# Kernel tuning notes

Hardware: AMD Instinct MI355X
Metric: run time of the kernel (lower is better)

The kernel has to match this reference:

```python
import jax, jax.numpy as jnp
import numpy as np

D_MODEL = 1024
NUM_HEADS = 16


def setup_inputs() -> dict:
    key = jax.random.key(0)
    ks = jax.random.split(key, 11)
    B, S, D = 2, 2048, D_MODEL
    s = 1.0 / np.sqrt(D)
    return {
        "queries": jax.random.normal(ks[0], (B, S, D), jnp.float32),
        "keys": jax.random.normal(ks[1], (B, S, D), jnp.float32),
        "values": jax.random.normal(ks[2], (B, S, D), jnp.float32),
        "W_q": jax.random.normal(ks[3], (D, D), jnp.float32) * s,
        "b_q": jnp.zeros((D,), jnp.float32),
        "W_k": jax.random.normal(ks[4], (D, D), jnp.float32) * s,
        "b_k": jnp.zeros((D,), jnp.float32),
        "W_v": jax.random.normal(ks[5], (D, D), jnp.float32) * s,
        "b_v": jnp.zeros((D,), jnp.float32),
        "W_o": jax.random.normal(ks[6], (D, D), jnp.float32) * s,
        "b_o": jnp.zeros((D,), jnp.float32),
    }


def _split_heads(x, num_heads):
    # [B, S, D] -> [B, H, S, d_h]
    B, S, D = x.shape
    return x.reshape(B, S, num_heads, D // num_heads).transpose(0, 2, 1, 3)


def reference(queries, keys, values, W_q, b_q, W_k, b_k, W_v, b_v, W_o, b_o):
    H = NUM_HEADS
    Q = _split_heads(queries @ W_q.T + b_q, H)  # [B,H,S,dh]
    K = _split_heads(keys @ W_k.T + b_k, H)
    V = _split_heads(values @ W_v.T + b_v, H)
    d = Q.shape[-1]
    scores = jnp.einsum("bhqd,bhkd->bhqk", Q, K) / jnp.sqrt(jnp.asarray(d, Q.dtype))
    attn = jax.nn.softmax(scores, axis=-1)
    out = jnp.einsum("bhqk,bhkd->bhqd", attn, V)  # [B,H,S,dh]
    B, _, S, _ = out.shape
    out = out.transpose(0, 2, 1, 3).reshape(B, S, -1)  # combine heads
    return out @ W_o.T + b_o
```

## Files before the change

### kernel.cpp

```cpp
#include <hip/hip_runtime.h>
#include <cstdint>
#include <cmath>

typedef short s16x8 __attribute__((ext_vector_type(8)));
typedef short s16x4 __attribute__((ext_vector_type(4)));
typedef float f32x4 __attribute__((ext_vector_type(4)));
typedef unsigned int u32;

#define AS_G __attribute__((address_space(1)))
#define AS_L __attribute__((address_space(3)))

#define QSCALE 0.18033688011112042f

__device__ __forceinline__ void ld16_to_lds(const void* g, const void* l) {
    __builtin_amdgcn_global_load_lds((AS_G void*)(g), (AS_L void*)(l), 16, 0, 0);
}

__device__ __forceinline__ short f2bf(float f) {
    union { float f; uint32_t u; } v; v.f = f;
    uint32_t r = v.u + 0x7fffu + ((v.u >> 16) & 1u);
    return (short)(r >> 16);
}
__device__ __forceinline__ short f2bf_fast(float f) {
    union { float f; uint32_t u; } v; v.f = f;
    return (short)((v.u + 0x8000u) >> 16);
}

template<int F32OUT, int NJ, int QKV>
__global__ __launch_bounds__(256, 3)
void gemm_bt(const short* __restrict__ Abase, long Az,
             const short* __restrict__ Wbase, long Wz,
             const float* __restrict__ bias0, const float* __restrict__ bias1,
             const float* __restrict__ bias2,
             void* __restrict__ Obase, long Oz,
             const int M, const int N, const int K)
{
    constexpr int BN = NJ * 32;
    constexpr int BSt = (BN * 4) / 256;
    constexpr int LPS = 2 + BSt;
    __shared__ __align__(16) short As[3][128 * 32];
    __shared__ __align__(16) short Bs[3][BN * 32];

    const int t = threadIdx.x, lane = t & 63, wv = t >> 6;
    const int wr = wv >> 1, wc = wv & 1;
    const int q4 = lane >> 4, l16 = lane & 15;

    const u32 gx = gridDim.x, gy = gridDim.y;
    u32 lin = blockIdx.x + gx * (blockIdx.y + gy * blockIdx.z);
    const u32 nwg = gx * gy * gridDim.z;
    if ((nwg & 7u) == 0u) lin = (lin & 7u) * (nwg >> 3) + (lin >> 3);
    const int bxs = lin % gx;
    const u32 rem = lin / gx;
    const int bys = rem % gy;
    const int z   = rem / gy;

    const short* A  = Abase + (long)z * Az;
    const short* Bt = Wbase + (long)z * Wz;
    const float* bias = (z == 0) ? bias0 : ((z == 1) ? bias1 : bias2);
    const float bmul = (QKV && z == 0) ? QSCALE : 1.0f;
    const int bn0 = bxs * BN, bm0 = bys * 128;

    f32x4 acc[4][NJ] = {};

    const short* gA[2];
    const short* gB[BSt];
    #pragma unroll
    for (int s = 0; s < 2; ++s) {
        const int c = t + 256 * s;
        const int r = c >> 2, g = (c & 3) ^ ((c >> 3) & 3);
        gA[s] = A + (size_t)(bm0 + r) * K + g * 8;
    }
    #pragma unroll
    for (int s = 0; s < BSt; ++s) {
        const int c = t + 256 * s;
        const int r = c >> 2, g = (c & 3) ^ ((c >> 3) & 3);
        gB[s] = Bt + (size_t)(bn0 + r) * K + g * 8;
    }

    auto stage = [&](int buf) {
        #pragma unroll
        for (int s = 0; s < 2; ++s) {
            ld16_to_lds(gA[s], &As[buf][(wv * 64 + 256 * s) * 8]);
            gA[s] += 32;
        }
        #pragma unroll
        for (int s = 0; s < BSt; ++s) {
            ld16_to_lds(gB[s], &Bs[buf][(wv * 64 + 256 * s) * 8]);
            gB[s] += 32;
        }
    };

    const int kIters = K >> 5;
    stage(0);
    stage(1);
    for (int kt = 0; kt < kIters; ++kt) {
        const int cur = kt % 3;
        if (kt < kIters - 1)
            asm volatile("s_waitcnt vmcnt(%0)" :: "n"(LPS) : "memory");
        else
            asm volatile("s_waitcnt vmcnt(0)" ::: "memory");
        __builtin_amdgcn_s_barrier();
        __builtin_amdgcn_sched_barrier(0);
        if (kt + 2 < kIters) stage((kt + 2) % 3);

        s16x8 aF[4], bF[NJ];
        #pragma unroll
        for (int i = 0; i < 4; ++i) {
            const int m = wr * 64 + i * 16 + l16;
            aF[i] = *(const s16x8*)&As[cur][m * 32 + (q4 ^ ((m >> 1) & 3)) * 8];
        }
        #pragma unroll
        for (int j = 0; j < NJ; ++j) {
            const int n = wc * (BN / 2) + j * 16 + l16;
            bF[j] = *(const s16x8*)&Bs[cur][n * 32 + (q4 ^ ((n >> 1) & 3)) * 8];
        }
        #pragma unroll
        for (int i = 0; i < 4; ++i)
            #pragma unroll
            for (int j = 0; j < NJ; ++j)
                acc[i][j] = __builtin_amdgcn_mfma_f32_16x16x32_bf16(
                    aF[i], bF[j], acc[i][j], 0, 0, 0);
    }

    #pragma unroll
    for (int j = 0; j < NJ; ++j) {
        const int col = bn0 + wc * (BN / 2) + j * 16 + l16;
        const float bj = bias[col] * bmul;
        #pragma unroll
        for (int i = 0; i < 4; ++i) {
            const int row0 = bm0 + wr * 64 + i * 16 + q4 * 4;
            if (QKV && z == 2) {
                s16x4 ov;
                #pragma unroll
                for (int r = 0; r < 4; ++r) ov[r] = f2bf(acc[i][j][r] + bj);
                *(s16x4*)(((short*)Obase + (long)z * Oz) +
                          (size_t)col * 4096 + row0) = ov;
            } else {
                #pragma unroll
                for (int r = 0; r < 4; ++r) {
                    const float v = acc[i][j][r] + bj;
                    if (F32OUT)
                        ((float*)Obase + (long)z * Oz)[(size_t)(row0 + r) * N + col] = v;
                    else
                        ((short*)Obase + (long)z * Oz)[(size_t)(row0 + r) * N + col] = f2bf(v);
                }
            }
        }
    }
}

__global__ __launch_bounds__(256, 2)
void attn_fwd(const short* __restrict__ Qp, const short* __restrict__ Kp,
              const short* __restrict__ VpT, short* __restrict__ Out)
{
    constexpr int D = 1024, S = 2048;
    __shared__ __align__(16) short Ks[2][512 * 8];
    __shared__ __align__(16) short Vt[2][512 * 8];
    __shared__ __align__(16) short Ps[4 * 32 * 72];

    const int t = threadIdx.x, lane = t & 63, wv = t >> 6;
    const int q4 = lane >> 4, l16 = lane & 15;
    const int bid = blockIdx.x;
    const int qt = (bid >> 3) & 15;
    const int hb = (bid & 7) * 4 + (bid >> 7);
    const int h = hb >> 1, b = hb & 1;
    const size_t rowB = (size_t)b * S;
    const int cb = h * 64;
    const int qrow0 = qt * 128 + wv * 32;
    short* PsW = &Ps[wv * (32 * 72)];

    const int ksrow = 4 * l16 + q4;

    s16x8 qF[2][2];
    #pragma unroll
    for (int i = 0; i < 2; ++i)
        #pragma unroll
        for (int tk = 0; tk < 2; ++tk)
            qF[i][tk] = *(const s16x8*)
                &Qp[(rowB + qrow0 + i * 16 + l16) * D + cb + tk * 32 + q4 * 8];

    f32x4 oacc[2][4] = {};
    f32x4 lacc[2] = {};
    s16x8 onesF;
    #pragma unroll
    for (int e = 0; e < 8; ++e) onesF[e] = (short)0x3F80;

    const short* KpB = Kp + rowB * D + cb;
    const short* VtG = VpT + (size_t)cb * 4096 + b * 2048;

    #pragma unroll
    for (int s = 0; s < 2; ++s) {
        ld16_to_lds(KpB + (size_t)ksrow * D + (wv + 4 * s) * 8,
                    &Ks[0][(wv * 64 + 256 * s) * 8]);
    }
    #pragma unroll
    for (int s = 0; s < 2; ++s) {
        const int c = t + 256 * s;
        const int d = c >> 3, kcp = c & 7;
        ld16_to_lds(VtG + (size_t)d * 4096 + ((kcp ^ (d & 7)) * 8),
                    &Vt[0][(wv * 64 + 256 * s) * 8]);
    }

    for (int kvt = 0; kvt < 32; ++kvt) {
        const int kv0 = kvt * 64;
        __syncthreads();
        if (kvt < 31) {
            #pragma unroll
            for (int s = 0; s < 2; ++s) {
                ld16_to_lds(KpB + (size_t)(kv0 + 64 + ksrow) * D + (wv + 4 * s) * 8,
                            &Ks[(kvt + 1) & 1][(wv * 64 + 256 * s) * 8]);
            }
            #pragma unroll
            for (int s = 0; s < 2; ++s) {
                const int c = t + 256 * s;
                const int d = c >> 3, kcp = c & 7;
                ld16_to_lds(VtG + (size_t)d * 4096 + kv0 + 64 + ((kcp ^ (d & 7)) * 8),
                            &Vt[(kvt + 1) & 1][(wv * 64 + 256 * s) * 8]);
            }
        }

        f32x4 acc[2][4] = {};
        #pragma unroll
        for (int tk = 0; tk < 2; ++tk) {
            s16x8 kF[4];
            #pragma unroll
            for (int j = 0; j < 4; ++j)
                kF[j] = *(const s16x8*)
                    &Ks[kvt & 1][((tk * 4 + q4) * 64 + j * 16 + l16) * 8];
            #pragma unroll
            for (int j = 0; j < 4; ++j) {
                acc[0][j] = __builtin_amdgcn_mfma_f32_16x16x32_bf16(
                    qF[0][tk], kF[j], acc[0][j], 0, 0, 0);
                acc[1][j] = __builtin_amdgcn_mfma_f32_16x16x32_bf16(
                    qF[1][tk], kF[j], acc[1][j], 0, 0, 0);
            }
        }

        #pragma unroll
        for (int i = 0; i < 2; ++i) {
            #pragma unroll
            for (int r = 0; r < 4; ++r) {
                const int m = i * 16 + q4 * 4 + r;
                s16x4 pv;
                #pragma unroll
                for (int j = 0; j < 4; ++j)
                    pv[j] = f2bf_fast(__builtin_amdgcn_exp2f(acc[i][j][r]));
                *(s16x4*)&PsW[m * 72 + l16 * 4] = pv;
            }
        }

        #pragma unroll
        for (int tk = 0; tk < 2; ++tk) {
            const s16x8 pF0 = *(const s16x8*)&PsW[l16 * 72 + tk * 32 + q4 * 8];
            const s16x8 pF1 = *(const s16x8*)&PsW[(16 + l16) * 72 + tk * 32 + q4 * 8];
            lacc[0] = __builtin_amdgcn_mfma_f32_16x16x32_bf16(
                pF0, onesF, lacc[0], 0, 0, 0);
            lacc[1] = __builtin_amdgcn_mfma_f32_16x16x32_bf16(
                pF1, onesF, lacc[1], 0, 0, 0);
            #pragma unroll
            for (int jd = 0; jd < 4; ++jd) {
                const int d = jd * 16 + l16;
                const s16x8 vF = *(const s16x8*)
                    &Vt[kvt & 1][(d * 8 + ((tk * 4 + q4) ^ (d & 7))) * 8];
                oacc[0][jd] = __builtin_amdgcn_mfma_f32_16x16x32_bf16(
                    pF0, vF, oacc[0][jd], 0, 0, 0);
                oacc[1][jd] = __builtin_amdgcn_mfma_f32_16x16x32_bf16(
                    pF1, vF, oacc[1][jd], 0, 0, 0);
            }
        }
    }

    #pragma unroll
    for (int i = 0; i < 2; ++i) {
        #pragma unroll
        for (int r = 0; r < 4; ++r) {
            const float inv = 1.0f / lacc[i][r];
            const size_t row = rowB + qrow0 + i * 16 + q4 * 4 + r;
            #pragma unroll
            for (int jd = 0; jd < 4; ++jd)
                Out[row * D + cb + jd * 16 + l16] = f2bf(oacc[i][jd][r] * inv);
        }
    }
}

__global__ __launch_bounds__(256)
void cast_all(const float* __restrict__ q, const float* __restrict__ k,
              const float* __restrict__ v, const float* __restrict__ wq,
              const float* __restrict__ wk, const float* __restrict__ wv,
              const float* __restrict__ wo, short* __restrict__ out)
{
    const size_t i = ((size_t)blockIdx.x * 256 + threadIdx.x) * 8;
    const float* src; size_t off;
    if      (i < 4194304)  { src = q;  off = i; }
    else if (i < 8388608)  { src = k;  off = i - 4194304; }
    else if (i < 12582912) { src = v;  off = i - 8388608; }
    else if (i < 13631488) { src = wq; off = i - 12582912; }
    else if (i < 14680064) { src = wk; off = i - 13631488; }
    else if (i < 15728640) { src = wv; off = i - 14680064; }
    else                   { src = wo; off = i - 15728640; }
    const float m = (i >= 12582912 && i < 13631488) ? QSCALE : 1.0f;
    const float4 a = *(const float4*)(src + off);
    const float4 c = *(const float4*)(src + off + 4);
    s16x8 o;
    o[0] = f2bf(a.x * m); o[1] = f2bf(a.y * m); o[2] = f2bf(a.z * m); o[3] = f2bf(a.w * m);
    o[4] = f2bf(c.x * m); o[5] = f2bf(c.y * m); o[6] = f2bf(c.z * m); o[7] = f2bf(c.w * m);
    *(s16x8*)(out + i) = o;
}

extern "C" void kernel_launch(void* const* d_in, const int* in_sizes, int n_in,
                              void* d_out, int out_size, void* d_ws, size_t ws_size,
                              hipStream_t stream)
{
    const float* q  = (const float*)d_in[0];
    const float* k  = (const float*)d_in[1];
    const float* v  = (const float*)d_in[2];
    const float* Wq = (const float*)d_in[3];
    const float* bq = (const float*)d_in[4];
    const float* Wk = (const float*)d_in[5];
    const float* bk = (const float*)d_in[6];
    const float* Wv = (const float*)d_in[7];
    const float* bv = (const float*)d_in[8];
    const float* Wo = (const float*)d_in[9];
    const float* bo = (const float*)d_in[10];

    short* ws = (short*)d_ws;
    const long MEL = 1048576;
    short* Aq  = ws;
    short* Wqb = ws + 12 * MEL;
    short* Wob = ws + 15 * MEL;
    short* Qp  = ws + 16 * MEL;
    short* Kp  = ws + 20 * MEL;
    short* VpT = ws + 24 * MEL;
    short* AO  = ws;

    cast_all<<<8192, 256, 0, stream>>>(q, k, v, Wq, Wk, Wv, Wo, ws);

    gemm_bt<0, 4, 1><<<dim3(8, 32, 3), 256, 0, stream>>>(
        Aq, 4 * MEL, Wqb, 1 * MEL, bq, bk, bv, Qp, 4 * MEL, 4096, 1024, 1024);

    attn_fwd<<<512, 256, 0, stream>>>(Qp, Kp, VpT, AO);

    gemm_bt<1, 2, 0><<<dim3(16, 32, 1), 256, 0, stream>>>(
        AO, 0, Wob, 0, bo, bo, bo, d_out, 0, 4096, 1024, 1024);
}
```

Measured before the change: 220.3 us.

## Halve attention query tile per wave, double grid, swizzle K/P LDS layouts

Each wave now handles 16 query rows instead of 32, so a block covers 64 queries and the grid doubles to 1024 blocks, with launch bounds raised to 4 blocks per CU. Register use drops because accumulators shrink by half, and P staging uses less LDS, which should allow higher occupancy to hide latency. K staging and the P scratch buffer switch from padded/strided layouts to XOR-swizzled layouts to avoid LDS bank conflicts. The cost is that each K/V tile loaded into LDS is reused by half as many query rows, which doubles K/V global traffic.

```diff
diff --git a/kernel.cpp b/kernel.cpp
--- a/kernel.cpp
+++ b/kernel.cpp
@@ -149,38 +149,34 @@
     }
 }
 
-__global__ __launch_bounds__(256, 2)
+__global__ __launch_bounds__(256, 4)
 void attn_fwd(const short* __restrict__ Qp, const short* __restrict__ Kp,
               const short* __restrict__ VpT, short* __restrict__ Out)
 {
     constexpr int D = 1024, S = 2048;
     __shared__ __align__(16) short Ks[2][512 * 8];
     __shared__ __align__(16) short Vt[2][512 * 8];
-    __shared__ __align__(16) short Ps[4 * 32 * 72];
+    __shared__ __align__(16) short Ps[4 * 16 * 64];
 
     const int t = threadIdx.x, lane = t & 63, wv = t >> 6;
     const int q4 = lane >> 4, l16 = lane & 15;
     const int bid = blockIdx.x;
-    const int qt = (bid >> 3) & 15;
-    const int hb = (bid & 7) * 4 + (bid >> 7);
+    const int qt = (bid >> 3) & 31;
+    const int hb = (bid & 7) * 4 + (bid >> 8);
     const int h = hb >> 1, b = hb & 1;
     const size_t rowB = (size_t)b * S;
     const int cb = h * 64;
-    const int qrow0 = qt * 128 + wv * 32;
-    short* PsW = &Ps[wv * (32 * 72)];
-
-    const int ksrow = 4 * l16 + q4;
-
-    s16x8 qF[2][2];
-    #pragma unroll
-    for (int i = 0; i < 2; ++i)
-        #pragma unroll
-        for (int tk = 0; tk < 2; ++tk)
-            qF[i][tk] = *(const s16x8*)
-                &Qp[(rowB + qrow0 + i * 16 + l16) * D + cb + tk * 32 + q4 * 8];
-
-    f32x4 oacc[2][4] = {};
-    f32x4 lacc[2] = {};
+    const int qrow0 = qt * 64 + wv * 16;
+    short* PsW = &Ps[wv * (16 * 64)];
+
+    s16x8 qF[2];
+    #pragma unroll
+    for (int tk = 0; tk < 2; ++tk)
+        qF[tk] = *(const s16x8*)
+            &Qp[(rowB + qrow0 + l16) * D + cb + tk * 32 + q4 * 8];
+
+    f32x4 oacc[4] = {};
+    f32x4 lacc = {};
     s16x8 onesF;
     #pragma unroll
     for (int e = 0; e < 8; ++e) onesF[e] = (short)0x3F80;
@@ -188,98 +184,81 @@
     const short* KpB = Kp + rowB * D + cb;
     const short* VtG = VpT + (size_t)cb * 4096 + b * 2048;
 
-    #pragma unroll
-    for (int s = 0; s < 2; ++s) {
-        ld16_to_lds(KpB + (size_t)ksrow * D + (wv + 4 * s) * 8,
-                    &Ks[0][(wv * 64 + 256 * s) * 8]);
-    }
-    #pragma unroll
-    for (int s = 0; s < 2; ++s) {
-        const int c = t + 256 * s;
-        const int d = c >> 3, kcp = c & 7;
-        ld16_to_lds(VtG + (size_t)d * 4096 + ((kcp ^ (d & 7)) * 8),
-                    &Vt[0][(wv * 64 + 256 * s) * 8]);
-    }
+    auto stageKV = [&](int buf, int kv0) {
+        #pragma unroll
+        for (int s = 0; s < 2; ++s) {
+            const int slot = (4 * s + wv) * 64 + lane;
+            const int r = slot >> 3;
+            const int kcs = (slot & 7) ^ ((r >> 2) & 7);
+            ld16_to_lds(KpB + (size_t)(kv0 + r) * D + kcs * 8,
+                        &Ks[buf][(wv * 64 + 256 * s) * 8]);
+        }
+        #pragma unroll
+        for (int s = 0; s < 2; ++s) {
+            const int c = t + 256 * s;
+            const int d = c >> 3, kcp = c & 7;
+            ld16_to_lds(VtG + (size_t)d * 4096 + kv0 + ((kcp ^ (d & 7)) * 8),
+                        &Vt[buf][(wv * 64 + 256 * s) * 8]);
+        }
+    };
+
+    stageKV(0, 0);
 
     for (int kvt = 0; kvt < 32; ++kvt) {
         const int kv0 = kvt * 64;
         __syncthreads();
-        if (kvt < 31) {
-            #pragma unroll
-            for (int s = 0; s < 2; ++s) {
-                ld16_to_lds(KpB + (size_t)(kv0 + 64 + ksrow) * D + (wv + 4 * s) * 8,
-                            &Ks[(kvt + 1) & 1][(wv * 64 + 256 * s) * 8]);
-            }
-            #pragma unroll
-            for (int s = 0; s < 2; ++s) {
-                const int c = t + 256 * s;
-                const int d = c >> 3, kcp = c & 7;
-                ld16_to_lds(VtG + (size_t)d * 4096 + kv0 + 64 + ((kcp ^ (d & 7)) * 8),
-                            &Vt[(kvt + 1) & 1][(wv * 64 + 256 * s) * 8]);
-            }
-        }
-
-        f32x4 acc[2][4] = {};
+        if (kvt < 31) stageKV((kvt + 1) & 1, kv0 + 64);
+
+        f32x4 acc[4] = {};
         #pragma unroll
         for (int tk = 0; tk < 2; ++tk) {
             s16x8 kF[4];
             #pragma unroll
             for (int j = 0; j < 4; ++j)
                 kF[j] = *(const s16x8*)
-                    &Ks[kvt & 1][((tk * 4 + q4) * 64 + j * 16 + l16) * 8];
-            #pragma unroll
-            for (int j = 0; j < 4; ++j) {
-                acc[0][j] = __builtin_amdgcn_mfma_f32_16x16x32_bf16(
-                    qF[0][tk], kF[j], acc[0][j], 0, 0, 0);
-                acc[1][j] = __builtin_amdgcn_mfma_f32_16x16x32_bf16(
-                    qF[1][tk], kF[j], acc[1][j], 0, 0, 0);
-            }
-        }
-
-        #pragma unroll
-        for (int i = 0; i < 2; ++i) {
-            #pragma unroll
-            for (int r = 0; r < 4; ++r) {
-                const int m = i * 16 + q4 * 4 + r;
-                s16x4 pv;
-                #pragma unroll
-                for (int j = 0; j < 4; ++j)
-                    pv[j] = f2bf_fast(__builtin_amdgcn_exp2f(acc[i][j][r]));
-                *(s16x4*)&PsW[m * 72 + l16 * 4] = pv;
-            }
+                    &Ks[kvt & 1][((4 * l16 + j) * 8 +
+                                  ((tk * 4 + q4) ^ (l16 & 7))) * 8];
+            #pragma unroll
+            for (int j = 0; j < 4; ++j)
+                acc[j] = __builtin_amdgcn_mfma_f32_16x16x32_bf16(
+                    qF[tk], kF[j], acc[j], 0, 0, 0);
+        }
+
+        #pragma unroll
+        for (int r = 0; r < 4; ++r) {
+            const int m = q4 * 4 + r;
+            s16x4 pv;
+            #pragma unroll
+            for (int j = 0; j < 4; ++j)
+                pv[j] = f2bf_fast(__builtin_amdgcn_exp2f(acc[j][r]));
+            *(s16x4*)((char*)PsW + m * 128 + ((l16 * 8) ^ ((m & 7) << 4))) = pv;
         }
 
         #pragma unroll
         for (int tk = 0; tk < 2; ++tk) {
-            const s16x8 pF0 = *(const s16x8*)&PsW[l16 * 72 + tk * 32 + q4 * 8];
-            const s16x8 pF1 = *(const s16x8*)&PsW[(16 + l16) * 72 + tk * 32 + q4 * 8];
-            lacc[0] = __builtin_amdgcn_mfma_f32_16x16x32_bf16(
-                pF0, onesF, lacc[0], 0, 0, 0);
-            lacc[1] = __builtin_amdgcn_mfma_f32_16x16x32_bf16(
-                pF1, onesF, lacc[1], 0, 0, 0);
+            const s16x8 pF = *(const s16x8*)
+                ((const char*)PsW + l16 * 128 +
+                 ((tk * 64 + q4 * 16) ^ ((l16 & 7) << 4)));
+            lacc = __builtin_amdgcn_mfma_f32_16x16x32_bf16(
+                pF, onesF, lacc, 0, 0, 0);
             #pragma unroll
             for (int jd = 0; jd < 4; ++jd) {
                 const int d = jd * 16 + l16;
                 const s16x8 vF = *(const s16x8*)
                     &Vt[kvt & 1][(d * 8 + ((tk * 4 + q4) ^ (d & 7))) * 8];
-                oacc[0][jd] = __builtin_amdgcn_mfma_f32_16x16x32_bf16(
-                    pF0, vF, oacc[0][jd], 0, 0, 0);
-                oacc[1][jd] = __builtin_amdgcn_mfma_f32_16x16x32_bf16(
-                    pF1, vF, oacc[1][jd], 0, 0, 0);
+                oacc[jd] = __builtin_amdgcn_mfma_f32_16x16x32_bf16(
+                    pF, vF, oacc[jd], 0, 0, 0);
             }
         }
     }
 
     #pragma unroll
-    for (int i = 0; i < 2; ++i) {
-        #pragma unroll
-        for (int r = 0; r < 4; ++r) {
-            const float inv = 1.0f / lacc[i][r];
-            const size_t row = rowB + qrow0 + i * 16 + q4 * 4 + r;
-            #pragma unroll
-            for (int jd = 0; jd < 4; ++jd)
-                Out[row * D + cb + jd * 16 + l16] = f2bf(oacc[i][jd][r] * inv);
-        }
+    for (int r = 0; r < 4; ++r) {
+        const float inv = 1.0f / lacc[r];
+        const size_t row = rowB + qrow0 + q4 * 4 + r;
+        #pragma unroll
+        for (int jd = 0; jd < 4; ++jd)
+            Out[row * D + cb + jd * 16 + l16] = f2bf(oacc[jd][r] * inv);
     }
 }
 
@@ -338,7 +317,7 @@
     gemm_bt<0, 4, 1><<<dim3(8, 32, 3), 256, 0, stream>>>(
         Aq, 4 * MEL, Wqb, 1 * MEL, bq, bk, bv, Qp, 4 * MEL, 4096, 1024, 1024);
 
-    attn_fwd<<<512, 256, 0, stream>>>(Qp, Kp, VpT, AO);
+    attn_fwd<<<1024, 256, 0, stream>>>(Qp, Kp, VpT, AO);
 
     gemm_bt<1, 2, 0><<<dim3(16, 32, 1), 256, 0, stream>>>(
         AO, 0, Wob, 0, bo, bo, bo, d_out, 0, 4096, 1024, 1024);
```

Measured after the change: 223.2 us. No clear change (+1.3%).
